# Performance work log

Measured on AMD Instinct MI355X. Metric: run time of the kernel, lower is better.

## Reference

```python
import jax, jax.numpy as jnp
import numpy as np

# dims: B=1, T=2048 (prefill), dim=3072, Hq=32, Hkv=8, D=128, S=max_seq_len=4096

def _rotate_interleave(x):
    # (-x1, x0, -x3, x2, ...) pairwise rotation on last dim
    x = x.reshape(x.shape[:-1] + (-1, 2))
    x = jnp.stack((-x[..., 1], x[..., 0]), axis=-1)
    return x.reshape(x.shape[:-2] + (-1,))


def setup_inputs() -> dict:
    key = jax.random.key(0)
    ks = jax.random.split(key, 8)
    B, T, DIM, HQ, HKV, HD, S = 1, 2048, 3072, 32, 8, 128, 4096
    x = jax.random.normal(ks[0], (B, T, DIM), jnp.float32)
    wq = jax.random.normal(ks[1], (HQ * HD, DIM), jnp.float32) * 0.02
    wk = jax.random.normal(ks[2], (HKV * HD, DIM), jnp.float32) * 0.02
    wv = jax.random.normal(ks[3], (HKV * HD, DIM), jnp.float32) * 0.02
    wo = jax.random.normal(ks[4], (DIM, HQ * HD), jnp.float32) * 0.02
    freqs_cos = jax.random.uniform(ks[5], (T, HD), jnp.float32)
    freqs_sin = jax.random.uniform(ks[6], (T, HD), jnp.float32)
    input_pos = jnp.zeros((1,), jnp.int32)
    k_cache = jnp.zeros((1, S, HKV, HD), jnp.float32)
    v_cache = jnp.zeros((1, S, HKV, HD), jnp.float32)
    return {"x": x, "wq": wq, "wk": wk, "wv": wv, "wo": wo,
            "freqs_cos": freqs_cos, "freqs_sin": freqs_sin,
            "k_cache": k_cache, "v_cache": v_cache, "input_pos": input_pos}


def reference(x, wq, wk, wv, wo, freqs_cos, freqs_sin, k_cache, v_cache, input_pos):
    B, T, _ = x.shape
    HQ, HKV, HD = 32, 8, 128
    q = (x @ wq.T).reshape(B, T, HQ, HD)
    k = (x @ wk.T).reshape(B, T, HKV, HD)
    v = (x @ wv.T).reshape(B, T, HKV, HD)
    # interleaved RoPE (computed in fp32 as in apply_rotary_emb)
    fc = freqs_cos[None, :, None, :]
    fs = freqs_sin[None, :, None, :]
    q = q * fc + _rotate_interleave(q) * fs
    k = k * fc + _rotate_interleave(k) * fs
    # KV-cache update at start_pos (torch.ops.llama.update_cache)
    sp = input_pos[0]
    k_all = jax.lax.dynamic_update_slice(k_cache, k, (0, sp, 0, 0))  # [1,S,HKV,HD]
    v_all = jax.lax.dynamic_update_slice(v_cache, v, (0, sp, 0, 0))
    S = k_all.shape[1]
    # GQA: expand kv heads to match q heads (head h -> kv head h // rep)
    rep = HQ // HKV
    kr = jnp.repeat(k_all, rep, axis=2)  # [1,S,HQ,HD]
    vr = jnp.repeat(v_all, rep, axis=2)
    scale = 1.0 / np.sqrt(HD).astype(np.float32)
    scores = jnp.einsum('bthd,bshd->bhts', q, kr) * scale  # [B,HQ,T,S]
    # causal mask relative to start_pos (custom_sdpa is_causal=True path)
    qpos = sp + jnp.arange(T)
    kpos = jnp.arange(S)
    mask = kpos[None, :] <= qpos[:, None]                   # [T,S]
    scores = jnp.where(mask[None, None], scores, jnp.float32(-1e30))
    attn = jax.nn.softmax(scores, axis=-1)
    y = jnp.einsum('bhts,bshd->bthd', attn, vr).reshape(B, T, HQ * HD)
    return y @ wo.T
```

## Files before the change

### kernel.cpp

```cpp
#include <hip/hip_runtime.h>
#include <hip/hip_bf16.h>
#include <stdint.h>

typedef float f32x4 __attribute__((ext_vector_type(4)));
typedef short s16x8 __attribute__((ext_vector_type(8)));
typedef short s16x4 __attribute__((ext_vector_type(4)));
typedef unsigned short u16x2 __attribute__((ext_vector_type(2)));
typedef unsigned short u16x4 __attribute__((ext_vector_type(4)));

#define AS1 __attribute__((address_space(1)))
#define AS3 __attribute__((address_space(3)))

static constexpr int T_    = 2048;
static constexpr int DIM_  = 3072;
static constexpr int HQ_   = 32;
static constexpr int HKV_  = 8;
static constexpr int HD_   = 128;
static constexpr int S_    = 4096;
static constexpr int NQKV_ = HQ_ * HD_ + 2 * HKV_ * HD_;

__device__ __forceinline__ unsigned short f2b(float f) {
  return __builtin_bit_cast(unsigned short, __float2bfloat16(f));
}
__device__ __forceinline__ float b2f(unsigned short u) {
  return __bfloat162float(__builtin_bit_cast(__hip_bfloat16, u));
}
__device__ __forceinline__ float exp2a(float x) {
  float r; asm("v_exp_f32 %0, %1" : "=v"(r) : "v"(x)); return r;
}

__device__ __forceinline__ void gld_lds16(const void* g, void* l) {
  __builtin_amdgcn_global_load_lds((AS1 unsigned int*)(uintptr_t)g,
                                   (AS3 unsigned int*)l, 16, 0, 0);
}

#define FENCE() asm volatile("" ::: "memory")
#define BAR()   do { FENCE(); __builtin_amdgcn_s_barrier(); FENCE(); } while (0)
#define WAIT_VM(n)   asm volatile("s_waitcnt vmcnt(" #n ")" ::: "memory")
#define WAIT_LGKM(n) asm volatile("s_waitcnt lgkmcnt(" #n ")" ::: "memory")
#define SCHEDB()     __builtin_amdgcn_sched_barrier(0)

__global__ __launch_bounds__(256)
void k_cvt(const float* __restrict__ src, unsigned short* __restrict__ dst, int n4) {
  int i = blockIdx.x * 256 + threadIdx.x;
  if (i >= n4) return;
  float4 v = reinterpret_cast<const float4*>(src)[i];
  u16x4 o;
  o.x = f2b(v.x); o.y = f2b(v.y); o.z = f2b(v.z); o.w = f2b(v.w);
  reinterpret_cast<u16x4*>(dst)[i] = o;
}

__global__ __launch_bounds__(256)
void k_cvtW(const float* __restrict__ wq, const float* __restrict__ wk,
            const float* __restrict__ wv, unsigned short* __restrict__ dst) {
  int idx = blockIdx.x * 256 + threadIdx.x;
  if (idx >= 4718592) return;
  const float* src; int s;
  if (idx < 3145728)      { src = wq; s = idx; }
  else if (idx < 3932160) { src = wk; s = idx - 3145728; }
  else                    { src = wv; s = idx - 3932160; }
  float4 v = reinterpret_cast<const float4*>(src)[s];
  u16x4 o;
  o.x = f2b(v.x); o.y = f2b(v.y); o.z = f2b(v.z); o.w = f2b(v.w);
  reinterpret_cast<u16x4*>(dst)[idx] = o;
}

template<int BMT, bool OUT_BF16>
__global__ __launch_bounds__(512, 4)
void k_gemm192(const unsigned short* __restrict__ A,
               const unsigned short* __restrict__ B,
               void* __restrict__ Cout, int N, int K, int KT,
               int nbn, int xcdq) {
  constexpr int AROWS  = BMT / 64;
  constexpr int AFRAG  = BMT / 32;
  constexpr int LDSBUF = BMT * 128 + 24576;
  __shared__ char lds[2 * LDSBUF];
  const int bid = blockIdx.x;
  const int swz = (bid & 7) * xcdq + (bid >> 3);
  const int bm  = swz / nbn, bn = swz % nbn;
  const int tid = threadIdx.x, lane = tid & 63, wid = tid >> 6;
  const int wm  = wid >> 2, wn = wid & 3;
  const int r16 = lane & 15, q4 = lane >> 4;

  const unsigned short* Ag = A + (size_t)(bm * BMT) * K;
  const unsigned short* Bg = B + (size_t)(bn * 192) * K;

  const int srow = tid >> 3;
  const int scol = ((tid & 7) ^ (srow & 7)) * 8;

  f32x4 acc[AFRAG][3] = {};
  s16x8 af[AFRAG][2];

  auto stageA = [&](int c, int r, int t) {
    gld_lds16(Ag + (size_t)(r * 64 + srow) * K + t * 64 + scol,
              lds + c * LDSBUF + r * 8192 + tid * 16);
  };
  auto stageB = [&](int c, int r, int t) {
    gld_lds16(Bg + (size_t)(r * 64 + srow) * K + t * 64 + scol,
              lds + c * LDSBUF + BMT * 128 + r * 8192 + tid * 16);
  };
  auto readA = [&](int c) {
    #pragma unroll
    for (int i = 0; i < AFRAG; ++i) {
      const int arow = wm * (BMT / 2) + i * 16 + r16;
      #pragma unroll
      for (int kk = 0; kk < 2; ++kk)
        af[i][kk] = *(const s16x8*)(lds + c * LDSBUF + arow * 128 +
                                    (((kk * 4 + q4) ^ (arow & 7)) << 4));
    }
  };
  auto readB = [&](s16x8 (&dst)[2], int c, int j) {
    const int brow = wn * 48 + j * 16 + r16;
    #pragma unroll
    for (int kk = 0; kk < 2; ++kk)
      dst[kk] = *(const s16x8*)(lds + c * LDSBUF + BMT * 128 + brow * 128 +
                                (((kk * 4 + q4) ^ (brow & 7)) << 4));
  };

#define MFMA8(BF, J)                                                           \
  __builtin_amdgcn_s_setprio(1);                                               \
  _Pragma("unroll")                                                            \
  for (int i_ = 0; i_ < AFRAG; ++i_) {                                         \
    _Pragma("unroll")                                                          \
    for (int kk_ = 0; kk_ < 2; ++kk_)                                          \
      acc[i_][J] = __builtin_amdgcn_mfma_f32_16x16x32_bf16(                    \
          af[i_][kk_], BF[kk_], acc[i_][J], 0, 0, 0);                          \
  }                                                                            \
  __builtin_amdgcn_s_setprio(0);

  #pragma unroll
  for (int r = 0; r < AROWS; ++r) stageA(0, r, 0);
  stageB(0, 0, 0); stageB(0, 1, 0); stageB(0, 2, 0);
  WAIT_VM(0);
  BAR();

  for (int t = 0; t < KT; ++t) {
    const int c = t & 1;
    const bool hn = (t + 1 < KT);
    s16x8 bf0[2], bf1[2], bf2[2];
    readA(c);
    readB(bf0, c, 0);
    if (hn) {
      #pragma unroll
      for (int r = 0; r < AROWS; ++r) stageA(c ^ 1, r, t + 1);
      stageB(c ^ 1, 0, t + 1); stageB(c ^ 1, 1, t + 1); stageB(c ^ 1, 2, t + 1);
    }
    readB(bf1, c, 1);
    WAIT_LGKM(2); SCHEDB();
    MFMA8(bf0, 0);
    readB(bf2, c, 2);
    WAIT_LGKM(2); SCHEDB();
    MFMA8(bf1, 1);
    WAIT_LGKM(0); SCHEDB();
    MFMA8(bf2, 2);
    if (hn) WAIT_VM(0);
    BAR();
  }
#undef MFMA8

  #pragma unroll
  for (int i = 0; i < AFRAG; ++i) {
    const int row = bm * BMT + wm * (BMT / 2) + i * 16 + q4 * 4;
    #pragma unroll
    for (int j = 0; j < 3; ++j) {
      const int col = bn * 192 + wn * 48 + j * 16 + r16;
      if constexpr (OUT_BF16) {
        unsigned short* C = (unsigned short*)Cout;
        #pragma unroll
        for (int rr = 0; rr < 4; ++rr)
          C[(size_t)(row + rr) * N + col] = f2b(acc[i][j][rr]);
      } else {
        float* C = (float*)Cout;
        #pragma unroll
        for (int rr = 0; rr < 4; ++rr)
          C[(size_t)(row + rr) * N + col] = acc[i][j][rr];
      }
    }
  }
}

__global__ __launch_bounds__(256)
void k_prep(const unsigned short* __restrict__ qkv,
            const float* __restrict__ fc, const float* __restrict__ fs,
            const float* __restrict__ kc, const float* __restrict__ vc,
            unsigned short* __restrict__ Qr, unsigned short* __restrict__ Kall,
            unsigned short* __restrict__ VT, const int* __restrict__ ipos) {
  __shared__ unsigned short lds[64][136];
  const int b = blockIdx.x, tid = threadIdx.x;

  if (b < 4096) {
    int idx = b * 256 + tid;
    int t   = idx >> 9;
    int rem = idx & 511;
    int h   = rem >> 4;
    int c8  = (rem & 15) << 3;
    s16x8 xv = *(const s16x8*)(qkv + (size_t)t * NQKV_ + h * HD_ + c8);
    float4 ca = *(const float4*)(fc + t * HD_ + c8);
    float4 cb = *(const float4*)(fc + t * HD_ + c8 + 4);
    float4 sa = *(const float4*)(fs + t * HD_ + c8);
    float4 sb = *(const float4*)(fs + t * HD_ + c8 + 4);
    float cc[8] = {ca.x, ca.y, ca.z, ca.w, cb.x, cb.y, cb.z, cb.w};
    float ss[8] = {sa.x, sa.y, sa.z, sa.w, sb.x, sb.y, sb.z, sb.w};
    s16x8 o;
    #pragma unroll
    for (int i = 0; i < 4; ++i) {
      float x0 = b2f((unsigned short)xv[2 * i]);
      float x1 = b2f((unsigned short)xv[2 * i + 1]);
      o[2 * i]     = (short)f2b(x0 * cc[2 * i]     - x1 * ss[2 * i]);
      o[2 * i + 1] = (short)f2b(x1 * cc[2 * i + 1] + x0 * ss[2 * i + 1]);
    }
    *(s16x8*)(Qr + ((size_t)h * T_ + t) * HD_ + c8) = o;

  } else if (b < 5120) {
    int idx = (b - 4096) * 256 + tid;
    int t   = idx >> 7;
    int rem = idx & 127;
    int hk  = rem >> 4;
    int c8  = (rem & 15) << 3;
    int sp  = ipos[0];
    s16x8 xv = *(const s16x8*)(qkv + (size_t)t * NQKV_ + HQ_ * HD_ + hk * HD_ + c8);
    float4 ca = *(const float4*)(fc + t * HD_ + c8);
    float4 cb = *(const float4*)(fc + t * HD_ + c8 + 4);
    float4 sa = *(const float4*)(fs + t * HD_ + c8);
    float4 sb = *(const float4*)(fs + t * HD_ + c8 + 4);
    float cc[8] = {ca.x, ca.y, ca.z, ca.w, cb.x, cb.y, cb.z, cb.w};
    float ss[8] = {sa.x, sa.y, sa.z, sa.w, sb.x, sb.y, sb.z, sb.w};
    s16x8 o;
    #pragma unroll
    for (int i = 0; i < 4; ++i) {
      float x0 = b2f((unsigned short)xv[2 * i]);
      float x1 = b2f((unsigned short)xv[2 * i + 1]);
      o[2 * i]     = (short)f2b(x0 * cc[2 * i]     - x1 * ss[2 * i]);
      o[2 * i + 1] = (short)f2b(x1 * cc[2 * i + 1] + x0 * ss[2 * i + 1]);
    }
    *(s16x8*)(Kall + ((size_t)hk * S_ + sp + t) * HD_ + c8) = o;

  } else if (b < 5376) {
    int bb = b - 5120;
    int hk = bb >> 5;
    int tt = bb & 31;
    int sp = ipos[0];
    #pragma unroll
    for (int p = 0; p < 4; ++p) {
      int e   = p * 256 + tid;
      int tr  = e >> 4;
      int col = (e & 15) << 3;
      *reinterpret_cast<s16x8*>(&lds[tr][col]) =
          *reinterpret_cast<const s16x8*>(&qkv[(size_t)(tt * 64 + tr) * NQKV_ +
                                               (HQ_ + HKV_) * HD_ + hk * HD_ + col]);
    }
    __syncthreads();
    #pragma unroll
    for (int p = 0; p < 32; ++p) {
      int e = p * 256 + tid;
      int d = e >> 6;
      int t = e & 63;
      VT[((size_t)hk * HD_ + d) * S_ + sp + tt * 64 + t] = lds[t][d];
    }

  } else {
    int sp = ipos[0];
    int total = sp * HKV_ * HD_;
    for (int idx = (b - 5376) * 256 + tid; idx < total; idx += 256 * 256) {
      int s   = idx >> 10;
      int rem = idx & 1023;
      int hk  = rem >> 7;
      int d   = rem & 127;
      Kall[((size_t)hk * S_ + s) * HD_ + d] = f2b(kc[((size_t)s * HKV_ + hk) * HD_ + d]);
      VT[((size_t)hk * HD_ + d) * S_ + s]   = f2b(vc[((size_t)s * HKV_ + hk) * HD_ + d]);
    }
  }
}

__global__ __launch_bounds__(256, 2)
void k_attn(const unsigned short* __restrict__ Qr,
            const unsigned short* __restrict__ Kall,
            const unsigned short* __restrict__ VT,
            unsigned short* __restrict__ Y,
            const int* __restrict__ ipos) {
  constexpr int QB = 64, KB = 64;
  __shared__ char lds[65536];
  const int bid  = blockIdx.x;
  const int hk   = bid & 7;
  const int j2   = bid >> 3;
  const int h    = hk * 4 + (j2 & 3);
  const int qt   = 31 - (j2 >> 2);
  const int tid  = threadIdx.x, lane = tid & 63, wave = tid >> 6;
  const int r16  = lane & 15, q4 = lane >> 4;
  const int vx   = r16 & 7;
  const float NEG_INF = -__builtin_inff();
  const float MINIT   = -1.0e30f;

  const int sp = ipos[0];
  const int qbase = qt * QB + wave * 16;
  const unsigned short* Kbase = Kall + (size_t)hk * S_ * HD_;
  const unsigned short* Vbase = VT + (size_t)hk * HD_ * S_;

  s16x8 qf[4];
  const unsigned short* qp = Qr + ((size_t)h * T_ + qbase + r16) * HD_;
  #pragma unroll
  for (int ki = 0; ki < 4; ++ki)
    qf[ki] = *reinterpret_cast<const s16x8*>(qp + ki * 32 + q4 * 8);
  SCHEDB(); WAIT_VM(0); SCHEDB();

  auto stage = [&](int c, int jt) {
    #pragma unroll
    for (int p = 0; p < 4; ++p) {
      int e  = p * 256 + tid;
      int kr = e >> 4;
      int ks = (e & 15) ^ (kr & 7);
      gld_lds16(Kbase + (size_t)(jt * KB + kr) * HD_ + ks * 8,
                lds + c * 16384 + e * 16);
    }
    #pragma unroll
    for (int p = 0; p < 4; ++p) {
      int e  = p * 256 + tid;
      int vd = e >> 3;
      int vs = (e & 7) ^ (vd & 7);
      gld_lds16(Vbase + (size_t)vd * S_ + jt * KB + vs * 8,
                lds + 32768 + c * 16384 + e * 16);
    }
  };

  f32x4 o[8] = {};
  float m = MINIT, l = 0.f;
  const int qpos = sp + qbase + r16;
  const int qpos_wave_max = sp + qbase + 15;
  int jmax = (sp + qt * QB + QB - 1) >> 6;
  if (jmax > S_ / KB - 1) jmax = S_ / KB - 1;
  const float scale2 = 0.12751744416312068f;

  stage(0, 0);

  for (int j = 0; j <= jmax; ++j) {
    const int c = j & 1;
    if (j < jmax) { stage(c ^ 1, j + 1); WAIT_VM(8); }
    else         { WAIT_VM(0); }
    BAR();

    const bool active = (j * KB <= qpos_wave_max);
    if (active) {
      const char* kb = lds + c * 16384;
      const char* vb = lds + 32768 + c * 16384;
      f32x4 sfr[4];
      __builtin_amdgcn_s_setprio(1);
      #pragma unroll
      for (int fn = 0; fn < 4; ++fn) {
        sfr[fn] = f32x4{0.f, 0.f, 0.f, 0.f};
        #pragma unroll
        for (int ki = 0; ki < 4; ++ki) {
          s16x8 kf = *(const s16x8*)(kb + (fn * 16 + r16) * 256 +
                                     (((ki * 4 + q4) ^ vx) << 4));
          sfr[fn] = __builtin_amdgcn_mfma_f32_16x16x32_bf16(kf, qf[ki], sfr[fn], 0, 0, 0);
        }
      }
      __builtin_amdgcn_s_setprio(0);
      float p[16];
      const bool needMask = (j * KB + KB - 1) > (sp + qbase);
      if (needMask) {
        const int kbp = j * KB + q4 * 4;
        #pragma unroll
        for (int fn = 0; fn < 4; ++fn)
          #pragma unroll
          for (int r = 0; r < 4; ++r)
            p[fn * 4 + r] = (kbp + fn * 16 + r <= qpos) ? sfr[fn][r] * scale2 : NEG_INF;
      } else {
        #pragma unroll
        for (int fn = 0; fn < 4; ++fn)
          #pragma unroll
          for (int r = 0; r < 4; ++r)
            p[fn * 4 + r] = sfr[fn][r] * scale2;
      }
      float t0 = fmaxf(p[0], p[1]),  t1 = fmaxf(p[2], p[3]);
      float t2 = fmaxf(p[4], p[5]),  t3 = fmaxf(p[6], p[7]);
      float t4 = fmaxf(p[8], p[9]),  t5 = fmaxf(p[10], p[11]);
      float t6 = fmaxf(p[12], p[13]), t7 = fmaxf(p[14], p[15]);
      float u0 = fmaxf(t0, t1), u1 = fmaxf(t2, t3);
      float u2 = fmaxf(t4, t5), u3 = fmaxf(t6, t7);
      float pmax = fmaxf(fmaxf(u0, u1), fmaxf(u2, u3));
      pmax = fmaxf(pmax, __shfl_xor(pmax, 16));
      pmax = fmaxf(pmax, __shfl_xor(pmax, 32));
      if (!__all(pmax <= m + 8.0f)) {
        float mn = fmaxf(m, pmax);
        float alpha = exp2a(m - mn);
        m = mn; l *= alpha;
        #pragma unroll
        for (int r = 0; r < 4; ++r) {
          float aq = __shfl(alpha, q4 * 4 + r);
          #pragma unroll
          for (int db = 0; db < 8; ++db) o[db][r] *= aq;
        }
      }
      float rs = 0.f;
      #pragma unroll
      for (int i = 0; i < 16; ++i) { p[i] = exp2a(p[i] - m); rs += p[i]; }
      rs += __shfl_xor(rs, 16); rs += __shfl_xor(rs, 32);
      l += rs;
      s16x8 pf[2];
      #pragma unroll
      for (int w = 0; w < 2; ++w)
        #pragma unroll
        for (int i = 0; i < 8; ++i)
          pf[w][i] = (short)f2b(p[w * 8 + i]);
      const int voff = (q4 & 1) * 8;
      const int sbase = q4 >> 1;
      __builtin_amdgcn_s_setprio(1);
      #pragma unroll
      for (int w = 0; w < 2; ++w) {
        #pragma unroll
        for (int db = 0; db < 8; ++db) {
          const char* vr = vb + (db * 16 + r16) * 128 + voff;
          s16x4 va = *(const s16x4*)(vr + (((w * 4 + sbase) ^ vx) << 4));
          s16x4 vb2 = *(const s16x4*)(vr + (((w * 4 + 2 + sbase) ^ vx) << 4));
          s16x8 vf = __builtin_shufflevector(va, vb2, 0, 1, 2, 3, 4, 5, 6, 7);
          o[db] = __builtin_amdgcn_mfma_f32_16x16x32_bf16(pf[w], vf, o[db], 0, 0, 0);
        }
      }
      __builtin_amdgcn_s_setprio(0);
    }
    BAR();
  }

  float rcpl = 1.0f / l;
  float rlq[4];
  #pragma unroll
  for (int r = 0; r < 4; ++r) rlq[r] = __shfl(rcpl, q4 * 4 + r);
  #pragma unroll
  for (int db = 0; db < 8; ++db)
    #pragma unroll
    for (int r = 0; r < 4; ++r) {
      int t = qt * QB + wave * 16 + q4 * 4 + r;
      int d = db * 16 + r16;
      Y[(size_t)t * (HQ_ * HD_) + h * HD_ + d] = f2b(o[db][r] * rlq[r]);
    }
}

extern "C" void kernel_launch(void* const* d_in, const int* in_sizes, int n_in,
                              void* d_out, int out_size, void* d_ws, size_t ws_size,
                              hipStream_t stream) {
  const float* x  = (const float*)d_in[0];
  const float* wq = (const float*)d_in[1];
  const float* wk = (const float*)d_in[2];
  const float* wv = (const float*)d_in[3];
  const float* wo = (const float*)d_in[4];
  const float* fc = (const float*)d_in[5];
  const float* fs = (const float*)d_in[6];
  const float* kc = (const float*)d_in[7];
  const float* vc = (const float*)d_in[8];
  const int* ipos = (const int*)d_in[9];

  char* ws = (char*)d_ws;
  unsigned short* xb   = (unsigned short*)(ws);
  unsigned short* wqkv = (unsigned short*)(ws + 12582912);
  unsigned short* qkv  = (unsigned short*)(ws + 50331648);
  unsigned short* Qr   = (unsigned short*)(ws + 75497472);
  unsigned short* Kall = (unsigned short*)(ws + 92274688);
  unsigned short* VT   = (unsigned short*)(ws + 100663296);
  unsigned short* wo_b = (unsigned short*)(ws);
  unsigned short* y    = qkv;

  k_cvt<<<6144, 256, 0, stream>>>(x, xb, 6291456 / 4);
  k_cvtW<<<18432, 256, 0, stream>>>(wq, wk, wv, wqkv);

  k_gemm192<128, true><<<512, 512, 0, stream>>>(xb, wqkv, qkv, NQKV_, DIM_, 48, 32, 64);

  k_cvt<<<12288, 256, 0, stream>>>(wo, wo_b, 12582912 / 4);

  k_prep<<<5632, 256, 0, stream>>>(qkv, fc, fs, kc, vc, Qr, Kall, VT, ipos);

  k_attn<<<1024, 256, 0, stream>>>(Qr, Kall, VT, y, ipos);

  k_gemm192<64, false><<<512, 512, 0, stream>>>(y, wo_b, d_out, DIM_, HQ_ * HD_, 64, 16, 64);
}
```

Before: 250.6 us.

## Fuse fp32-to-bf16 weight conversion into GEMM B-operand staging

The separate conversion kernels for the QKV and output-projection weights are removed. Both GEMMs now load fp32 weight rows straight into registers, convert them to bf16 and write them into swizzled LDS, with the three QKV weight matrices selected by row range. This avoids writing and re-reading a bf16 copy of the weights and saves two launches. The cost is more global traffic per tile, since every M-block re-reads fp32 weights, plus register staging and conversion ALU work inside the main loop in place of async direct-to-LDS loads.

```diff
diff --git a/kernel.cpp b/kernel.cpp
--- a/kernel.cpp
+++ b/kernel.cpp
@@ -50,25 +50,11 @@
   reinterpret_cast<u16x4*>(dst)[i] = o;
 }
 
-__global__ __launch_bounds__(256)
-void k_cvtW(const float* __restrict__ wq, const float* __restrict__ wk,
-            const float* __restrict__ wv, unsigned short* __restrict__ dst) {
-  int idx = blockIdx.x * 256 + threadIdx.x;
-  if (idx >= 4718592) return;
-  const float* src; int s;
-  if (idx < 3145728)      { src = wq; s = idx; }
-  else if (idx < 3932160) { src = wk; s = idx - 3145728; }
-  else                    { src = wv; s = idx - 3932160; }
-  float4 v = reinterpret_cast<const float4*>(src)[s];
-  u16x4 o;
-  o.x = f2b(v.x); o.y = f2b(v.y); o.z = f2b(v.z); o.w = f2b(v.w);
-  reinterpret_cast<u16x4*>(dst)[idx] = o;
-}
-
 template<int BMT, bool OUT_BF16>
 __global__ __launch_bounds__(512, 4)
 void k_gemm192(const unsigned short* __restrict__ A,
-               const unsigned short* __restrict__ B,
+               const float* __restrict__ B0, const float* __restrict__ B1,
+               const float* __restrict__ B2, int rb1, int rb2,
                void* __restrict__ Cout, int N, int K, int KT,
                int nbn, int xcdq) {
   constexpr int AROWS  = BMT / 64;
@@ -83,21 +69,49 @@
   const int r16 = lane & 15, q4 = lane >> 4;
 
   const unsigned short* Ag = A + (size_t)(bm * BMT) * K;
-  const unsigned short* Bg = B + (size_t)(bn * 192) * K;
 
   const int srow = tid >> 3;
   const int scol = ((tid & 7) ^ (srow & 7)) * 8;
 
+  const float* bptr[3];
+  int wds[3];
+  #pragma unroll
+  for (int i = 0; i < 3; ++i) {
+    int e    = i * 512 + tid;
+    int row  = e >> 3, slot = e & 7;
+    int rg   = bn * 192 + row;
+    const float* bp = (rg < rb1) ? B0 + (size_t)rg * K
+                    : (rg < rb2) ? B1 + (size_t)(rg - rb1) * K
+                                 : B2 + (size_t)(rg - rb2) * K;
+    bptr[i] = bp + slot * 8;
+    wds[i]  = BMT * 128 + row * 128 + ((slot ^ (row & 7)) << 4);
+  }
+
   f32x4 acc[AFRAG][3] = {};
   s16x8 af[AFRAG][2];
+  float4 br[3][2];
 
   auto stageA = [&](int c, int r, int t) {
     gld_lds16(Ag + (size_t)(r * 64 + srow) * K + t * 64 + scol,
               lds + c * LDSBUF + r * 8192 + tid * 16);
   };
-  auto stageB = [&](int c, int r, int t) {
-    gld_lds16(Bg + (size_t)(r * 64 + srow) * K + t * 64 + scol,
-              lds + c * LDSBUF + BMT * 128 + r * 8192 + tid * 16);
+  auto loadB = [&](int t) {
+    #pragma unroll
+    for (int i = 0; i < 3; ++i) {
+      br[i][0] = *(const float4*)(bptr[i] + t * 64);
+      br[i][1] = *(const float4*)(bptr[i] + t * 64 + 4);
+    }
+  };
+  auto cvtWriteB = [&](int c) {
+    #pragma unroll
+    for (int i = 0; i < 3; ++i) {
+      s16x8 o;
+      o[0] = (short)f2b(br[i][0].x); o[1] = (short)f2b(br[i][0].y);
+      o[2] = (short)f2b(br[i][0].z); o[3] = (short)f2b(br[i][0].w);
+      o[4] = (short)f2b(br[i][1].x); o[5] = (short)f2b(br[i][1].y);
+      o[6] = (short)f2b(br[i][1].z); o[7] = (short)f2b(br[i][1].w);
+      *(s16x8*)(lds + c * LDSBUF + wds[i]) = o;
+    }
   };
   auto readA = [&](int c) {
     #pragma unroll
@@ -128,23 +142,25 @@
   }                                                                            \
   __builtin_amdgcn_s_setprio(0);
 
+  loadB(0);
   #pragma unroll
   for (int r = 0; r < AROWS; ++r) stageA(0, r, 0);
-  stageB(0, 0, 0); stageB(0, 1, 0); stageB(0, 2, 0);
   WAIT_VM(0);
+  cvtWriteB(0);
+  WAIT_LGKM(0);
   BAR();
 
   for (int t = 0; t < KT; ++t) {
     const int c = t & 1;
     const bool hn = (t + 1 < KT);
     s16x8 bf0[2], bf1[2], bf2[2];
+    if (hn) {
+      loadB(t + 1);
+      #pragma unroll
+      for (int r = 0; r < AROWS; ++r) stageA(c ^ 1, r, t + 1);
+    }
     readA(c);
     readB(bf0, c, 0);
-    if (hn) {
-      #pragma unroll
-      for (int r = 0; r < AROWS; ++r) stageA(c ^ 1, r, t + 1);
-      stageB(c ^ 1, 0, t + 1); stageB(c ^ 1, 1, t + 1); stageB(c ^ 1, 2, t + 1);
-    }
     readB(bf1, c, 1);
     WAIT_LGKM(2); SCHEDB();
     MFMA8(bf0, 0);
@@ -153,7 +169,11 @@
     MFMA8(bf1, 1);
     WAIT_LGKM(0); SCHEDB();
     MFMA8(bf2, 2);
-    if (hn) WAIT_VM(0);
+    if (hn) {
+      WAIT_VM(0);
+      cvtWriteB(c ^ 1);
+      WAIT_LGKM(0);
+    }
     BAR();
   }
 #undef MFMA8
@@ -451,24 +471,21 @@
 
   char* ws = (char*)d_ws;
   unsigned short* xb   = (unsigned short*)(ws);
-  unsigned short* wqkv = (unsigned short*)(ws + 12582912);
   unsigned short* qkv  = (unsigned short*)(ws + 50331648);
   unsigned short* Qr   = (unsigned short*)(ws + 75497472);
   unsigned short* Kall = (unsigned short*)(ws + 92274688);
   unsigned short* VT   = (unsigned short*)(ws + 100663296);
-  unsigned short* wo_b = (unsigned short*)(ws);
   unsigned short* y    = qkv;
 
   k_cvt<<<6144, 256, 0, stream>>>(x, xb, 6291456 / 4);
-  k_cvtW<<<18432, 256, 0, stream>>>(wq, wk, wv, wqkv);
-
-  k_gemm192<128, true><<<512, 512, 0, stream>>>(xb, wqkv, qkv, NQKV_, DIM_, 48, 32, 64);
-
-  k_cvt<<<12288, 256, 0, stream>>>(wo, wo_b, 12582912 / 4);
+
+  k_gemm192<128, true><<<512, 512, 0, stream>>>(xb, wq, wk, wv, 4096, 5120,
+                                                qkv, NQKV_, DIM_, 48, 32, 64);
 
   k_prep<<<5632, 256, 0, stream>>>(qkv, fc, fs, kc, vc, Qr, Kall, VT, ipos);
 
   k_attn<<<1024, 256, 0, stream>>>(Qr, Kall, VT, y, ipos);
 
-  k_gemm192<64, false><<<512, 512, 0, stream>>>(y, wo_b, d_out, DIM_, HQ_ * HD_, 64, 16, 64);
-}
+  k_gemm192<64, false><<<512, 512, 0, stream>>>(y, wo, wo, wo, 1 << 30, 1 << 30,
+                                                d_out, DIM_, HQ_ * HD_, 64, 16, 64);
+}
```

Result: slower. 409.1 us (+63.3%).

## Process two GQA query heads per attention block to share staged K/V tiles

Applied to the files above, without the earlier changes.

Each attention workgroup now handles two query heads that share one KV head, reusing each K/V tile staged in LDS for both heads and halving the grid to 512 blocks. This cuts global-to-LDS traffic and barrier count per unit of work. The cost is doubled accumulator and Q-fragment registers, which may hurt occupancy under the 2-waves launch bound. Fewer blocks also means coarser load balance across the causal triangle.

```diff
diff --git a/kernel.cpp b/kernel.cpp
--- a/kernel.cpp
+++ b/kernel.cpp
@@ -282,9 +282,10 @@
   __shared__ char lds[65536];
   const int bid  = blockIdx.x;
   const int hk   = bid & 7;
-  const int j2   = bid >> 3;
-  const int h    = hk * 4 + (j2 & 3);
-  const int qt   = 31 - (j2 >> 2);
+  const int u    = bid >> 3;
+  const int pr   = u & 1;
+  const int qt   = 31 - (u >> 1);
+  const int h0   = hk * 4 + pr * 2;
   const int tid  = threadIdx.x, lane = tid & 63, wave = tid >> 6;
   const int r16  = lane & 15, q4 = lane >> 4;
   const int vx   = r16 & 7;
@@ -296,11 +297,16 @@
   const unsigned short* Kbase = Kall + (size_t)hk * S_ * HD_;
   const unsigned short* Vbase = VT + (size_t)hk * HD_ * S_;
 
-  s16x8 qf[4];
-  const unsigned short* qp = Qr + ((size_t)h * T_ + qbase + r16) * HD_;
-  #pragma unroll
-  for (int ki = 0; ki < 4; ++ki)
-    qf[ki] = *reinterpret_cast<const s16x8*>(qp + ki * 32 + q4 * 8);
+  s16x8 qf0[4], qf1[4];
+  {
+    const unsigned short* qp0 = Qr + ((size_t)h0 * T_ + qbase + r16) * HD_;
+    const unsigned short* qp1 = qp0 + (size_t)T_ * HD_;
+    #pragma unroll
+    for (int ki = 0; ki < 4; ++ki) {
+      qf0[ki] = *reinterpret_cast<const s16x8*>(qp0 + ki * 32 + q4 * 8);
+      qf1[ki] = *reinterpret_cast<const s16x8*>(qp1 + ki * 32 + q4 * 8);
+    }
+  }
   SCHEDB(); WAIT_VM(0); SCHEDB();
 
   auto stage = [&](int c, int jt) {
@@ -322,8 +328,8 @@
     }
   };
 
-  f32x4 o[8] = {};
-  float m = MINIT, l = 0.f;
+  f32x4 o0[8] = {}, o1[8] = {};
+  float m0 = MINIT, l0 = 0.f, m1 = MINIT, l1 = 0.f;
   const int qpos = sp + qbase + r16;
   const int qpos_wave_max = sp + qbase + 15;
   int jmax = (sp + qt * QB + QB - 1) >> 6;
@@ -342,97 +348,109 @@
     if (active) {
       const char* kb = lds + c * 16384;
       const char* vb = lds + 32768 + c * 16384;
-      f32x4 sfr[4];
-      __builtin_amdgcn_s_setprio(1);
+      const bool needMask = (j * KB + KB - 1) > (sp + qbase);
+
+      auto headPass = [&](const s16x8 (&qf)[4], f32x4 (&o)[8],
+                          float& m, float& l) {
+        f32x4 sfr[4];
+        __builtin_amdgcn_s_setprio(1);
+        #pragma unroll
+        for (int fn = 0; fn < 4; ++fn) {
+          sfr[fn] = f32x4{0.f, 0.f, 0.f, 0.f};
+          #pragma unroll
+          for (int ki = 0; ki < 4; ++ki) {
+            s16x8 kf = *(const s16x8*)(kb + (fn * 16 + r16) * 256 +
+                                       (((ki * 4 + q4) ^ vx) << 4));
+            sfr[fn] = __builtin_amdgcn_mfma_f32_16x16x32_bf16(kf, qf[ki], sfr[fn], 0, 0, 0);
+          }
+        }
+        __builtin_amdgcn_s_setprio(0);
+        float p[16];
+        if (needMask) {
+          const int kbp = j * KB + q4 * 4;
+          #pragma unroll
+          for (int fn = 0; fn < 4; ++fn)
+            #pragma unroll
+            for (int r = 0; r < 4; ++r)
+              p[fn * 4 + r] = (kbp + fn * 16 + r <= qpos) ? sfr[fn][r] * scale2 : NEG_INF;
+        } else {
+          #pragma unroll
+          for (int fn = 0; fn < 4; ++fn)
+            #pragma unroll
+            for (int r = 0; r < 4; ++r)
+              p[fn * 4 + r] = sfr[fn][r] * scale2;
+        }
+        float t0 = fmaxf(p[0], p[1]),  t1 = fmaxf(p[2], p[3]);
+        float t2 = fmaxf(p[4], p[5]),  t3 = fmaxf(p[6], p[7]);
+        float t4 = fmaxf(p[8], p[9]),  t5 = fmaxf(p[10], p[11]);
+        float t6 = fmaxf(p[12], p[13]), t7 = fmaxf(p[14], p[15]);
+        float pmax = fmaxf(fmaxf(fmaxf(t0, t1), fmaxf(t2, t3)),
+                           fmaxf(fmaxf(t4, t5), fmaxf(t6, t7)));
+        pmax = fmaxf(pmax, __shfl_xor(pmax, 16));
+        pmax = fmaxf(pmax, __shfl_xor(pmax, 32));
+        if (!__all(pmax <= m + 8.0f)) {
+          float mn = fmaxf(m, pmax);
+          float alpha = exp2a(m - mn);
+          m = mn; l *= alpha;
+          #pragma unroll
+          for (int r = 0; r < 4; ++r) {
+            float aq = __shfl(alpha, q4 * 4 + r);
+            #pragma unroll
+            for (int db = 0; db < 8; ++db) o[db][r] *= aq;
+          }
+        }
+        float rs = 0.f;
+        #pragma unroll
+        for (int i = 0; i < 16; ++i) { p[i] = exp2a(p[i] - m); rs += p[i]; }
+        rs += __shfl_xor(rs, 16); rs += __shfl_xor(rs, 32);
+        l += rs;
+        s16x8 pf[2];
+        #pragma unroll
+        for (int w = 0; w < 2; ++w)
+          #pragma unroll
+          for (int i = 0; i < 8; ++i)
+            pf[w][i] = (short)f2b(p[w * 8 + i]);
+        const int voff = (q4 & 1) * 8;
+        const int sbase = q4 >> 1;
+        __builtin_amdgcn_s_setprio(1);
+        #pragma unroll
+        for (int w = 0; w < 2; ++w) {
+          #pragma unroll
+          for (int db = 0; db < 8; ++db) {
+            const char* vr = vb + (db * 16 + r16) * 128 + voff;
+            s16x4 va  = *(const s16x4*)(vr + (((w * 4 + sbase) ^ vx) << 4));
+            s16x4 vb2 = *(const s16x4*)(vr + (((w * 4 + 2 + sbase) ^ vx) << 4));
+            s16x8 vf = __builtin_shufflevector(va, vb2, 0, 1, 2, 3, 4, 5, 6, 7);
+            o[db] = __builtin_amdgcn_mfma_f32_16x16x32_bf16(pf[w], vf, o[db], 0, 0, 0);
+          }
+        }
+        __builtin_amdgcn_s_setprio(0);
+      };
+
+      headPass(qf0, o0, m0, l0);
+      headPass(qf1, o1, m1, l1);
+    }
+    BAR();
+  }
+
+  {
+    float rcpl0 = 1.0f / l0, rcpl1 = 1.0f / l1;
+    float rl0[4], rl1[4];
+    #pragma unroll
+    for (int r = 0; r < 4; ++r) {
+      rl0[r] = __shfl(rcpl0, q4 * 4 + r);
+      rl1[r] = __shfl(rcpl1, q4 * 4 + r);
+    }
+    #pragma unroll
+    for (int db = 0; db < 8; ++db)
       #pragma unroll
-      for (int fn = 0; fn < 4; ++fn) {
-        sfr[fn] = f32x4{0.f, 0.f, 0.f, 0.f};
-        #pragma unroll
-        for (int ki = 0; ki < 4; ++ki) {
-          s16x8 kf = *(const s16x8*)(kb + (fn * 16 + r16) * 256 +
-                                     (((ki * 4 + q4) ^ vx) << 4));
-          sfr[fn] = __builtin_amdgcn_mfma_f32_16x16x32_bf16(kf, qf[ki], sfr[fn], 0, 0, 0);
-        }
+      for (int r = 0; r < 4; ++r) {
+        int t = qt * QB + wave * 16 + q4 * 4 + r;
+        int d = db * 16 + r16;
+        Y[(size_t)t * (HQ_ * HD_) + h0 * HD_ + d]       = f2b(o0[db][r] * rl0[r]);
+        Y[(size_t)t * (HQ_ * HD_) + (h0 + 1) * HD_ + d] = f2b(o1[db][r] * rl1[r]);
       }
-      __builtin_amdgcn_s_setprio(0);
-      float p[16];
-      const bool needMask = (j * KB + KB - 1) > (sp + qbase);
-      if (needMask) {
-        const int kbp = j * KB + q4 * 4;
-        #pragma unroll
-        for (int fn = 0; fn < 4; ++fn)
-          #pragma unroll
-          for (int r = 0; r < 4; ++r)
-            p[fn * 4 + r] = (kbp + fn * 16 + r <= qpos) ? sfr[fn][r] * scale2 : NEG_INF;
-      } else {
-        #pragma unroll
-        for (int fn = 0; fn < 4; ++fn)
-          #pragma unroll
-          for (int r = 0; r < 4; ++r)
-            p[fn * 4 + r] = sfr[fn][r] * scale2;
-      }
-      float t0 = fmaxf(p[0], p[1]),  t1 = fmaxf(p[2], p[3]);
-      float t2 = fmaxf(p[4], p[5]),  t3 = fmaxf(p[6], p[7]);
-      float t4 = fmaxf(p[8], p[9]),  t5 = fmaxf(p[10], p[11]);
-      float t6 = fmaxf(p[12], p[13]), t7 = fmaxf(p[14], p[15]);
-      float u0 = fmaxf(t0, t1), u1 = fmaxf(t2, t3);
-      float u2 = fmaxf(t4, t5), u3 = fmaxf(t6, t7);
-      float pmax = fmaxf(fmaxf(u0, u1), fmaxf(u2, u3));
-      pmax = fmaxf(pmax, __shfl_xor(pmax, 16));
-      pmax = fmaxf(pmax, __shfl_xor(pmax, 32));
-      if (!__all(pmax <= m + 8.0f)) {
-        float mn = fmaxf(m, pmax);
-        float alpha = exp2a(m - mn);
-        m = mn; l *= alpha;
-        #pragma unroll
-        for (int r = 0; r < 4; ++r) {
-          float aq = __shfl(alpha, q4 * 4 + r);
-          #pragma unroll
-          for (int db = 0; db < 8; ++db) o[db][r] *= aq;
-        }
-      }
-      float rs = 0.f;
-      #pragma unroll
-      for (int i = 0; i < 16; ++i) { p[i] = exp2a(p[i] - m); rs += p[i]; }
-      rs += __shfl_xor(rs, 16); rs += __shfl_xor(rs, 32);
-      l += rs;
-      s16x8 pf[2];
-      #pragma unroll
-      for (int w = 0; w < 2; ++w)
-        #pragma unroll
-        for (int i = 0; i < 8; ++i)
-          pf[w][i] = (short)f2b(p[w * 8 + i]);
-      const int voff = (q4 & 1) * 8;
-      const int sbase = q4 >> 1;
-      __builtin_amdgcn_s_setprio(1);
-      #pragma unroll
-      for (int w = 0; w < 2; ++w) {
-        #pragma unroll
-        for (int db = 0; db < 8; ++db) {
-          const char* vr = vb + (db * 16 + r16) * 128 + voff;
-          s16x4 va = *(const s16x4*)(vr + (((w * 4 + sbase) ^ vx) << 4));
-          s16x4 vb2 = *(const s16x4*)(vr + (((w * 4 + 2 + sbase) ^ vx) << 4));
-          s16x8 vf = __builtin_shufflevector(va, vb2, 0, 1, 2, 3, 4, 5, 6, 7);
-          o[db] = __builtin_amdgcn_mfma_f32_16x16x32_bf16(pf[w], vf, o[db], 0, 0, 0);
-        }
-      }
-      __builtin_amdgcn_s_setprio(0);
-    }
-    BAR();
-  }
-
-  float rcpl = 1.0f / l;
-  float rlq[4];
-  #pragma unroll
-  for (int r = 0; r < 4; ++r) rlq[r] = __shfl(rcpl, q4 * 4 + r);
-  #pragma unroll
-  for (int db = 0; db < 8; ++db)
-    #pragma unroll
-    for (int r = 0; r < 4; ++r) {
-      int t = qt * QB + wave * 16 + q4 * 4 + r;
-      int d = db * 16 + r16;
-      Y[(size_t)t * (HQ_ * HD_) + h * HD_ + d] = f2b(o[db][r] * rlq[r]);
-    }
+  }
 }
 
 extern "C" void kernel_launch(void* const* d_in, const int* in_sizes, int n_in,
@@ -468,7 +486,7 @@
 
   k_prep<<<5632, 256, 0, stream>>>(qkv, fc, fs, kc, vc, Qr, Kall, VT, ipos);
 
-  k_attn<<<1024, 256, 0, stream>>>(Qr, Kall, VT, y, ipos);
+  k_attn<<<512, 256, 0, stream>>>(Qr, Kall, VT, y, ipos);
 
   k_gemm192<64, false><<<512, 512, 0, stream>>>(y, wo_b, d_out, DIM_, HQ_ * HD_, 64, 16, 64);
 }
```

Result: slower. 280.9 us (+12.1%).

## Fuse conversion kernels and apply Q RoPE inside attention kernel

Applied to the files above, without the earlier changes.

Merges the x and QKV-weight fp32→bf16 conversions into one launch, and folds the wo conversion into the prep kernel, cutting two kernel launches. Q rotary embedding is no longer written to a separate Qr buffer; the attention kernel now loads raw Q from the qkv buffer plus cos/sin and rotates it in registers. This removes a full write and read of Q. The cost is more scattered global loads at the start of attention, and y now gets its own buffer.

```diff
diff --git a/kernel.cpp b/kernel.cpp
--- a/kernel.cpp
+++ b/kernel.cpp
@@ -41,28 +41,26 @@
 #define SCHEDB()     __builtin_amdgcn_sched_barrier(0)
 
 __global__ __launch_bounds__(256)
-void k_cvt(const float* __restrict__ src, unsigned short* __restrict__ dst, int n4) {
-  int i = blockIdx.x * 256 + threadIdx.x;
-  if (i >= n4) return;
-  float4 v = reinterpret_cast<const float4*>(src)[i];
-  u16x4 o;
-  o.x = f2b(v.x); o.y = f2b(v.y); o.z = f2b(v.z); o.w = f2b(v.w);
-  reinterpret_cast<u16x4*>(dst)[i] = o;
-}
-
-__global__ __launch_bounds__(256)
-void k_cvtW(const float* __restrict__ wq, const float* __restrict__ wk,
-            const float* __restrict__ wv, unsigned short* __restrict__ dst) {
+void k_cvtA(const float* __restrict__ x,  const float* __restrict__ wq,
+            const float* __restrict__ wk, const float* __restrict__ wv,
+            unsigned short* __restrict__ xb, unsigned short* __restrict__ wqkv) {
   int idx = blockIdx.x * 256 + threadIdx.x;
-  if (idx >= 4718592) return;
-  const float* src; int s;
-  if (idx < 3145728)      { src = wq; s = idx; }
-  else if (idx < 3932160) { src = wk; s = idx - 3145728; }
-  else                    { src = wv; s = idx - 3932160; }
-  float4 v = reinterpret_cast<const float4*>(src)[s];
-  u16x4 o;
-  o.x = f2b(v.x); o.y = f2b(v.y); o.z = f2b(v.z); o.w = f2b(v.w);
-  reinterpret_cast<u16x4*>(dst)[idx] = o;
+  if (idx < 1572864) {
+    float4 v = reinterpret_cast<const float4*>(x)[idx];
+    u16x4 o;
+    o.x = f2b(v.x); o.y = f2b(v.y); o.z = f2b(v.z); o.w = f2b(v.w);
+    reinterpret_cast<u16x4*>(xb)[idx] = o;
+  } else {
+    int j = idx - 1572864;
+    const float* src; int s;
+    if (j < 3145728)      { src = wq; s = j; }
+    else if (j < 3932160) { src = wk; s = j - 3145728; }
+    else                  { src = wv; s = j - 3932160; }
+    float4 v = reinterpret_cast<const float4*>(src)[s];
+    u16x4 o;
+    o.x = f2b(v.x); o.y = f2b(v.y); o.z = f2b(v.z); o.w = f2b(v.w);
+    reinterpret_cast<u16x4*>(wqkv)[j] = o;
+  }
 }
 
 template<int BMT, bool OUT_BF16>
@@ -183,36 +181,21 @@
 void k_prep(const unsigned short* __restrict__ qkv,
             const float* __restrict__ fc, const float* __restrict__ fs,
             const float* __restrict__ kc, const float* __restrict__ vc,
-            unsigned short* __restrict__ Qr, unsigned short* __restrict__ Kall,
+            const float* __restrict__ wo, unsigned short* __restrict__ wo_b,
+            unsigned short* __restrict__ Kall,
             unsigned short* __restrict__ VT, const int* __restrict__ ipos) {
   __shared__ unsigned short lds[64][136];
   const int b = blockIdx.x, tid = threadIdx.x;
 
-  if (b < 4096) {
+  if (b < 12288) {
     int idx = b * 256 + tid;
-    int t   = idx >> 9;
-    int rem = idx & 511;
-    int h   = rem >> 4;
-    int c8  = (rem & 15) << 3;
-    s16x8 xv = *(const s16x8*)(qkv + (size_t)t * NQKV_ + h * HD_ + c8);
-    float4 ca = *(const float4*)(fc + t * HD_ + c8);
-    float4 cb = *(const float4*)(fc + t * HD_ + c8 + 4);
-    float4 sa = *(const float4*)(fs + t * HD_ + c8);
-    float4 sb = *(const float4*)(fs + t * HD_ + c8 + 4);
-    float cc[8] = {ca.x, ca.y, ca.z, ca.w, cb.x, cb.y, cb.z, cb.w};
-    float ss[8] = {sa.x, sa.y, sa.z, sa.w, sb.x, sb.y, sb.z, sb.w};
-    s16x8 o;
-    #pragma unroll
-    for (int i = 0; i < 4; ++i) {
-      float x0 = b2f((unsigned short)xv[2 * i]);
-      float x1 = b2f((unsigned short)xv[2 * i + 1]);
-      o[2 * i]     = (short)f2b(x0 * cc[2 * i]     - x1 * ss[2 * i]);
-      o[2 * i + 1] = (short)f2b(x1 * cc[2 * i + 1] + x0 * ss[2 * i + 1]);
-    }
-    *(s16x8*)(Qr + ((size_t)h * T_ + t) * HD_ + c8) = o;
-
-  } else if (b < 5120) {
-    int idx = (b - 4096) * 256 + tid;
+    float4 v = reinterpret_cast<const float4*>(wo)[idx];
+    u16x4 o;
+    o.x = f2b(v.x); o.y = f2b(v.y); o.z = f2b(v.z); o.w = f2b(v.w);
+    reinterpret_cast<u16x4*>(wo_b)[idx] = o;
+
+  } else if (b < 13312) {
+    int idx = (b - 12288) * 256 + tid;
     int t   = idx >> 7;
     int rem = idx & 127;
     int hk  = rem >> 4;
@@ -235,8 +218,8 @@
     }
     *(s16x8*)(Kall + ((size_t)hk * S_ + sp + t) * HD_ + c8) = o;
 
-  } else if (b < 5376) {
-    int bb = b - 5120;
+  } else if (b < 13568) {
+    int bb = b - 13312;
     int hk = bb >> 5;
     int tt = bb & 31;
     int sp = ipos[0];
@@ -261,7 +244,7 @@
   } else {
     int sp = ipos[0];
     int total = sp * HKV_ * HD_;
-    for (int idx = (b - 5376) * 256 + tid; idx < total; idx += 256 * 256) {
+    for (int idx = (b - 13568) * 256 + tid; idx < total; idx += 256 * 256) {
       int s   = idx >> 10;
       int rem = idx & 1023;
       int hk  = rem >> 7;
@@ -273,7 +256,8 @@
 }
 
 __global__ __launch_bounds__(256, 2)
-void k_attn(const unsigned short* __restrict__ Qr,
+void k_attn(const unsigned short* __restrict__ qkv,
+            const float* __restrict__ fc, const float* __restrict__ fs,
             const unsigned short* __restrict__ Kall,
             const unsigned short* __restrict__ VT,
             unsigned short* __restrict__ Y,
@@ -297,10 +281,30 @@
   const unsigned short* Vbase = VT + (size_t)hk * HD_ * S_;
 
   s16x8 qf[4];
-  const unsigned short* qp = Qr + ((size_t)h * T_ + qbase + r16) * HD_;
-  #pragma unroll
-  for (int ki = 0; ki < 4; ++ki)
-    qf[ki] = *reinterpret_cast<const s16x8*>(qp + ki * 32 + q4 * 8);
+  {
+    const int tq = qbase + r16;
+    const unsigned short* qp = qkv + (size_t)tq * NQKV_ + h * HD_;
+    const float* fcb = fc + tq * HD_;
+    const float* fsb = fs + tq * HD_;
+    #pragma unroll
+    for (int ki = 0; ki < 4; ++ki) {
+      const int d0 = ki * 32 + q4 * 8;
+      s16x8 xv = *reinterpret_cast<const s16x8*>(qp + d0);
+      float4 ca = *(const float4*)(fcb + d0);
+      float4 cb = *(const float4*)(fcb + d0 + 4);
+      float4 sa = *(const float4*)(fsb + d0);
+      float4 sb = *(const float4*)(fsb + d0 + 4);
+      float cc[8] = {ca.x, ca.y, ca.z, ca.w, cb.x, cb.y, cb.z, cb.w};
+      float ss[8] = {sa.x, sa.y, sa.z, sa.w, sb.x, sb.y, sb.z, sb.w};
+      #pragma unroll
+      for (int i = 0; i < 4; ++i) {
+        float x0 = b2f((unsigned short)xv[2 * i]);
+        float x1 = b2f((unsigned short)xv[2 * i + 1]);
+        qf[ki][2 * i]     = (short)f2b(x0 * cc[2 * i]     - x1 * ss[2 * i]);
+        qf[ki][2 * i + 1] = (short)f2b(x1 * cc[2 * i + 1] + x0 * ss[2 * i + 1]);
+      }
+    }
+  }
   SCHEDB(); WAIT_VM(0); SCHEDB();
 
   auto stage = [&](int c, int jt) {
@@ -375,9 +379,8 @@
       float t2 = fmaxf(p[4], p[5]),  t3 = fmaxf(p[6], p[7]);
       float t4 = fmaxf(p[8], p[9]),  t5 = fmaxf(p[10], p[11]);
       float t6 = fmaxf(p[12], p[13]), t7 = fmaxf(p[14], p[15]);
-      float u0 = fmaxf(t0, t1), u1 = fmaxf(t2, t3);
-      float u2 = fmaxf(t4, t5), u3 = fmaxf(t6, t7);
-      float pmax = fmaxf(fmaxf(u0, u1), fmaxf(u2, u3));
+      float pmax = fmaxf(fmaxf(fmaxf(t0, t1), fmaxf(t2, t3)),
+                         fmaxf(fmaxf(t4, t5), fmaxf(t6, t7)));
       pmax = fmaxf(pmax, __shfl_xor(pmax, 16));
       pmax = fmaxf(pmax, __shfl_xor(pmax, 32));
       if (!__all(pmax <= m + 8.0f)) {
@@ -410,7 +413,7 @@
         #pragma unroll
         for (int db = 0; db < 8; ++db) {
           const char* vr = vb + (db * 16 + r16) * 128 + voff;
-          s16x4 va = *(const s16x4*)(vr + (((w * 4 + sbase) ^ vx) << 4));
+          s16x4 va  = *(const s16x4*)(vr + (((w * 4 + sbase) ^ vx) << 4));
           s16x4 vb2 = *(const s16x4*)(vr + (((w * 4 + 2 + sbase) ^ vx) << 4));
           s16x8 vf = __builtin_shufflevector(va, vb2, 0, 1, 2, 3, 4, 5, 6, 7);
           o[db] = __builtin_amdgcn_mfma_f32_16x16x32_bf16(pf[w], vf, o[db], 0, 0, 0);
@@ -453,22 +456,18 @@
   unsigned short* xb   = (unsigned short*)(ws);
   unsigned short* wqkv = (unsigned short*)(ws + 12582912);
   unsigned short* qkv  = (unsigned short*)(ws + 50331648);
-  unsigned short* Qr   = (unsigned short*)(ws + 75497472);
+  unsigned short* y    = (unsigned short*)(ws + 75497472);
   unsigned short* Kall = (unsigned short*)(ws + 92274688);
   unsigned short* VT   = (unsigned short*)(ws + 100663296);
   unsigned short* wo_b = (unsigned short*)(ws);
-  unsigned short* y    = qkv;
-
-  k_cvt<<<6144, 256, 0, stream>>>(x, xb, 6291456 / 4);
-  k_cvtW<<<18432, 256, 0, stream>>>(wq, wk, wv, wqkv);
+
+  k_cvtA<<<24576, 256, 0, stream>>>(x, wq, wk, wv, xb, wqkv);
 
   k_gemm192<128, true><<<512, 512, 0, stream>>>(xb, wqkv, qkv, NQKV_, DIM_, 48, 32, 64);
 
-  k_cvt<<<12288, 256, 0, stream>>>(wo, wo_b, 12582912 / 4);
-
-  k_prep<<<5632, 256, 0, stream>>>(qkv, fc, fs, kc, vc, Qr, Kall, VT, ipos);
-
-  k_attn<<<1024, 256, 0, stream>>>(Qr, Kall, VT, y, ipos);
+  k_prep<<<13824, 256, 0, stream>>>(qkv, fc, fs, kc, vc, wo, wo_b, Kall, VT, ipos);
+
+  k_attn<<<1024, 256, 0, stream>>>(qkv, fc, fs, Kall, VT, y, ipos);
 
   k_gemm192<64, false><<<512, 512, 0, stream>>>(y, wo_b, d_out, DIM_, HQ_ * HD_, 64, 16, 64);
 }
```

Result: no change. 248.5 us (-0.8%).
